# Performance work log

Hardware: AMD Instinct MI355X
Metric: run time of the kernel (lower is better)

The kernel has to match this reference:

```python
import jax, jax.numpy as jnp
import numpy as np

D = 2048
G = 16


def setup_inputs() -> dict:
    key = jax.random.key(0)
    ks = jax.random.split(key, 7)
    scale = 1.0 / np.sqrt(D)
    x = jax.random.normal(ks[0], (4, 4096, D), dtype=jnp.float32)
    Wq = jax.random.uniform(ks[1], (D, D), jnp.float32, -scale, scale)
    bq = jax.random.uniform(ks[2], (D,), jnp.float32, -scale, scale)
    Wk = jax.random.uniform(ks[3], (D, D), jnp.float32, -scale, scale)
    bk = jax.random.uniform(ks[4], (D,), jnp.float32, -scale, scale)
    Wv = jax.random.uniform(ks[5], (D, D), jnp.float32, -scale, scale)
    bv = jax.random.uniform(ks[6], (D,), jnp.float32, -scale, scale)
    return {"x": x, "Wq": Wq, "bq": bq, "Wk": Wk, "bk": bk, "Wv": Wv, "bv": bv}


def reference(x, Wq, bq, Wk, bk, Wv, bv):
    B, T, Df = x.shape
    g = G
    d = Df // g  # per-group dim = 128
    q = x @ Wq.T + bq
    k = x @ Wk.T + bk
    v = x @ Wv.T + bv
    qs = q.reshape(B, T, g, d)
    ks_ = k.reshape(B, T, g, d)
    vs = v.reshape(B, T, g, d)
    # attention over the GROUP axis per token: scores are (B,T,g,g)
    scores = jnp.einsum('btgd,bthd->btgh', qs, ks_) / jnp.sqrt(jnp.asarray(d, x.dtype))
    att = jax.nn.softmax(scores, axis=-1)
    out = jnp.einsum('btgh,bthd->btgd', att, vs)
    return out.reshape(B, T, Df)
```

## Files before the change

kernel.cpp:

```cpp
#include <hip/hip_runtime.h>


#define DIM 2048
#define NTOT 6144
#define DG 128
#define NG 16
#define BK 64
#define KT64 (DIM / BK)

typedef __bf16 bf16x8 __attribute__((ext_vector_type(8)));
typedef float f32x4 __attribute__((ext_vector_type(4)));
typedef unsigned short u16;
typedef unsigned int u32;

__device__ __forceinline__ u16 f2bf(float f) {
  u32 u = __float_as_uint(f);
  u = (u + 0x7fffu + ((u >> 16) & 1u)) >> 16;
  return (u16)u;
}

__device__ __forceinline__ void gload16(const __bf16* g, __bf16* l) {
  __builtin_amdgcn_global_load_lds(
      (__attribute__((address_space(1))) void*)(void*)g,
      (__attribute__((address_space(3))) void*)l, 16, 0, 0);
}

__global__ __launch_bounds__(256) void cvt_kernel(const float* __restrict__ src,
                                                  u16* __restrict__ dst, int n4) {
  int i = blockIdx.x * 256 + threadIdx.x;
  if (i >= n4) return;
  float4 f = ((const float4*)src)[i];
  ushort4 o;
  o.x = f2bf(f.x); o.y = f2bf(f.y); o.z = f2bf(f.z); o.w = f2bf(f.w);
  ((ushort4*)dst)[i] = o;
}

__global__ __launch_bounds__(256) void cvtW_kernel(const float* __restrict__ wq,
                                                   const float* __restrict__ wk,
                                                   const float* __restrict__ wv,
                                                   u16* __restrict__ dst, int n4each) {
  int m = blockIdx.y;
  const float* s = (m == 0) ? wq : (m == 1) ? wk : wv;
  int i = blockIdx.x * 256 + threadIdx.x;
  if (i >= n4each) return;
  float4 f = ((const float4*)s)[i];
  ushort4 o;
  o.x = f2bf(f.x); o.y = f2bf(f.y); o.z = f2bf(f.z); o.w = f2bf(f.w);
  ((ushort4*)dst)[(size_t)m * n4each + i] = o;
}

__global__ __launch_bounds__(512, 1) void gemm_qkv(const __bf16* __restrict__ A,
                                                   const __bf16* __restrict__ W,
                                                   const float* __restrict__ bq,
                                                   const float* __restrict__ bk,
                                                   const float* __restrict__ bv,
                                                   u16* __restrict__ C) {
  __shared__ __bf16 lds[2 * 32768];

  const int tid = threadIdx.x;
  const int lane = tid & 63;
  const int w = tid >> 6;
  const int wm = w >> 2, wn = w & 3;
  const int lm = lane & 15, kq = lane >> 4;

  const int bid = blockIdx.x;
  const int swz = (bid & 7) * 192 + (bid >> 3);
  const int bm = swz % 64;
  const int bn = swz / 64;

  const int srow = tid >> 3;
  const int scol = ((tid & 7) ^ ((tid >> 3) & 7)) * 8;
  const __bf16* pA = A + (size_t)(bm * 256 + srow) * DIM + scol;
  const __bf16* pB = W + (size_t)(bn * 256 + srow) * DIM + scol;

#define STAGEH(tt, p)                                                         \
  {                                                                           \
    __bf16* db = lds + ((tt) & 1) * 32768 + ((p) >> 1) * 16384 +              \
                 ((p) & 1) * 8192 + tid * 8;                                  \
    const __bf16* sp = (((p) >> 1) == 0 ? pA : pB) +                          \
                       (size_t)(((p) & 1) * 128) * DIM + (size_t)(tt) * BK;   \
    gload16(sp, db);                                                          \
    gload16(sp + (size_t)64 * DIM, db + 4096);                                \
  }

  f32x4 acc[8][4];
#pragma unroll
  for (int i = 0; i < 8; ++i)
#pragma unroll
    for (int j = 0; j < 4; ++j) acc[i][j] = (f32x4){0.f, 0.f, 0.f, 0.f};

  int aoff[2][2], boff[2][2];
#pragma unroll
  for (int ih = 0; ih < 2; ++ih)
#pragma unroll
    for (int kk = 0; kk < 2; ++kk)
      aoff[ih][kk] = (wm * 128 + ih * 64 + lm) * 64 + (((kk << 2) | kq) ^ (lm & 7)) * 8;
#pragma unroll
  for (int jh = 0; jh < 2; ++jh)
#pragma unroll
    for (int kk = 0; kk < 2; ++kk)
      boff[jh][kk] = (wn * 64 + jh * 32 + lm) * 64 + (((kk << 2) | kq) ^ (lm & 7)) * 8;

  bf16x8 af[4][2], bfr[2][2];

#define PH(tv, ih, jh, dostage, p)                                            \
  {                                                                           \
    const __bf16* bufb = lds + ((tv) & 1) * 32768;                            \
    if ((jh) == 0) {                                                          \
      _Pragma("unroll") for (int ir = 0; ir < 4; ++ir)                        \
        _Pragma("unroll") for (int kk = 0; kk < 2; ++kk)                      \
          af[ir][kk] = *(const bf16x8*)(bufb + aoff[ih][kk] + ir * 1024);     \
    }                                                                         \
    _Pragma("unroll") for (int jr = 0; jr < 2; ++jr)                          \
      _Pragma("unroll") for (int kk = 0; kk < 2; ++kk)                        \
        bfr[jr][kk] = *(const bf16x8*)(bufb + 16384 + boff[jh][kk] + jr * 1024); \
    if (dostage) STAGEH((tv) + 1, p);                                         \
    __builtin_amdgcn_sched_barrier(0);                                       \
    asm volatile("s_barrier" ::: "memory");                                   \
    asm volatile("s_waitcnt lgkmcnt(0)" ::: "memory");                        \
    __builtin_amdgcn_sched_barrier(0);                                       \
    __builtin_amdgcn_s_setprio(1);                                            \
    _Pragma("unroll") for (int ir = 0; ir < 4; ++ir)                          \
      _Pragma("unroll") for (int jr = 0; jr < 2; ++jr)                        \
        _Pragma("unroll") for (int kk = 0; kk < 2; ++kk)                      \
          acc[(ih) * 4 + ir][(jh) * 2 + jr] =                                 \
              __builtin_amdgcn_mfma_f32_16x16x32_bf16(                        \
                  af[ir][kk], bfr[jr][kk], acc[(ih) * 4 + ir][(jh) * 2 + jr], \
                  0, 0, 0);                                                   \
    __builtin_amdgcn_s_setprio(0);                                            \
    if ((p) == 3) asm volatile("s_waitcnt vmcnt(0)" ::: "memory");            \
    asm volatile("s_barrier" ::: "memory");                                   \
  }

  STAGEH(0, 0) STAGEH(0, 1) STAGEH(0, 2) STAGEH(0, 3)
  asm volatile("s_waitcnt vmcnt(0)" ::: "memory");
  asm volatile("s_barrier" ::: "memory");

#pragma unroll 1
  for (int t = 0; t < KT64 - 1; ++t) {
    PH(t, 0, 0, 1, 0)
    PH(t, 0, 1, 1, 1)
    PH(t, 1, 0, 1, 2)
    PH(t, 1, 1, 1, 3)
  }
  PH(KT64 - 1, 0, 0, 0, 0)
  PH(KT64 - 1, 0, 1, 0, 1)
  PH(KT64 - 1, 1, 0, 0, 2)
  PH(KT64 - 1, 1, 1, 0, 3)
#undef PH
#undef STAGEH

  const int mat = bn >> 3;
  const float* bias = (mat == 0) ? bq : (mat == 1) ? bk : bv;
  const int colb = bn * 256 + wn * 64 + lm;
  const int rowb = bm * 256 + wm * 128 + kq * 4;
#pragma unroll
  for (int i = 0; i < 8; ++i) {
#pragma unroll
    for (int j = 0; j < 4; ++j) {
      const int col = colb + j * 16;
      const float bs = bias[col & (DIM - 1)];
#pragma unroll
      for (int r = 0; r < 4; ++r) {
        const int row = rowb + i * 16 + r;
        C[(size_t)row * NTOT + col] = f2bf(acc[i][j][r] + bs);
      }
    }
  }
}

__device__ __forceinline__ void unpack8(uint4 v, float* f) {
  f[0] = __uint_as_float(v.x << 16);
  f[1] = __uint_as_float(v.x & 0xffff0000u);
  f[2] = __uint_as_float(v.y << 16);
  f[3] = __uint_as_float(v.y & 0xffff0000u);
  f[4] = __uint_as_float(v.z << 16);
  f[5] = __uint_as_float(v.z & 0xffff0000u);
  f[6] = __uint_as_float(v.w << 16);
  f[7] = __uint_as_float(v.w & 0xffff0000u);
}

__global__ __launch_bounds__(256) void attn_kernel(const u16* __restrict__ qkv,
                                                   float* __restrict__ out) {
  __shared__ __bf16 kv[4][4096];

  const int tid = threadIdx.x;
  const int lane = tid & 63;
  const int w = tid >> 6;
  const int token = blockIdx.x * 4 + w;
  const int g = lane & 15, s = lane >> 4;

  const __bf16* base = (const __bf16*)(qkv) + (size_t)token * NTOT;

  const __bf16* kvsrc = base + DIM;
#pragma unroll
  for (int i = 0; i < 8; ++i)
    gload16(kvsrc + i * 512 + lane * 8, (__bf16*)kv[w] + i * 512);

  float qf[32];
  const __bf16* qsrc = base + g * DG + s * 32;
#pragma unroll
  for (int j = 0; j < 4; ++j) {
    uint4 qc = *(const uint4*)(qsrc + j * 8);
    unpack8(qc, qf + j * 8);
  }

  asm volatile("s_waitcnt vmcnt(0)" ::: "memory");

  float sc[16];
  const __bf16* kl = (const __bf16*)kv[w] + s * 32;
#pragma unroll 4
  for (int h = 0; h < 16; ++h) {
    const uint4* kr = (const uint4*)(kl + h * DG);
    float a = 0.f;
#pragma unroll
    for (int j = 0; j < 4; ++j) {
      float kf[8];
      unpack8(kr[j], kf);
#pragma unroll
      for (int e = 0; e < 8; ++e) a = fmaf(qf[j * 8 + e], kf[e], a);
    }
    sc[h] = a;
  }
#pragma unroll
  for (int h = 0; h < 16; ++h) {
    float v = sc[h];
    v += __shfl_xor(v, 16);
    v += __shfl_xor(v, 32);
    sc[h] = v;
  }

  const float scale = 0.08838834764831845f;
  float mx = sc[0] * scale;
#pragma unroll
  for (int h = 1; h < 16; ++h) mx = fmaxf(mx, sc[h] * scale);
  float p[16], sum = 0.f;
#pragma unroll
  for (int h = 0; h < 16; ++h) {
    p[h] = __expf(sc[h] * scale - mx);
    sum += p[h];
  }
  const float inv = 1.f / sum;
#pragma unroll
  for (int h = 0; h < 16; ++h) p[h] *= inv;

  float o[32];
#pragma unroll
  for (int e = 0; e < 32; ++e) o[e] = 0.f;
  const __bf16* vl = (const __bf16*)kv[w] + 2048 + s * 32;
#pragma unroll 4
  for (int h = 0; h < 16; ++h) {
    const uint4* vr = (const uint4*)(vl + h * DG);
    const float ph = p[h];
#pragma unroll
    for (int j = 0; j < 4; ++j) {
      float vf[8];
      unpack8(vr[j], vf);
#pragma unroll
      for (int e = 0; e < 8; ++e) o[j * 8 + e] = fmaf(ph, vf[e], o[j * 8 + e]);
    }
  }

  float* ob = out + (size_t)token * DIM + g * DG + s * 32;
#pragma unroll
  for (int j = 0; j < 8; ++j) {
    float4 v4 = {o[j * 4], o[j * 4 + 1], o[j * 4 + 2], o[j * 4 + 3]};
    ((float4*)ob)[j] = v4;
  }
}

extern "C" void kernel_launch(void* const* d_in, const int* in_sizes, int n_in,
                              void* d_out, int out_size, void* d_ws, size_t ws_size,
                              hipStream_t stream) {
  const float* x  = (const float*)d_in[0];
  const float* Wq = (const float*)d_in[1];
  const float* bq = (const float*)d_in[2];
  const float* Wk = (const float*)d_in[3];
  const float* bk = (const float*)d_in[4];
  const float* Wv = (const float*)d_in[5];
  const float* bv = (const float*)d_in[6];
  float* out = (float*)d_out;

  const int M = in_sizes[0] / DIM;

  u16* xb  = (u16*)d_ws;
  u16* wb  = xb + (size_t)M * DIM;
  u16* qkv = wb + (size_t)3 * DIM * DIM;

  const int n4x = (M * DIM) / 4;
  cvt_kernel<<<dim3((n4x + 255) / 256), 256, 0, stream>>>(x, xb, n4x);
  const int n4w = (DIM * DIM) / 4;
  cvtW_kernel<<<dim3((n4w + 255) / 256, 3), 256, 0, stream>>>(Wq, Wk, Wv, wb, n4w);

  gemm_qkv<<<dim3((M / 256) * (NTOT / 256)), 512, 0, stream>>>(
      (const __bf16*)xb, (const __bf16*)wb, bq, bk, bv, qkv);

  attn_kernel<<<dim3(M / 4), 256, 0, stream>>>(qkv, out);
}
```

Measured before the change: 719.7 us.

## Split LDS tiles into K-halves to wait on partial loads earlier

Restructures the QKV GEMM's shared-memory staging so each 64-wide K tile is stored as two 32-wide halves (A and B each), with a new XOR swizzle for 32-element rows. Each phase now handles one K-half and one row half with the full 4x4 MFMA set. The loop waits with vmcnt(4) instead of vmcnt(0), so compute on the first K-half can start while the second half is still in flight. The intent is finer-grained overlap of global-to-LDS copies with MFMA. The vmcnt bookkeeping is delicate, and the wait count and swizzle must match the load order exactly.

```diff
diff --git a/kernel.cpp b/kernel.cpp
--- a/kernel.cpp
+++ b/kernel.cpp
@@ -68,19 +68,17 @@
   const int bm = swz % 64;
   const int bn = swz / 64;
 
-  const int srow = tid >> 3;
-  const int scol = ((tid & 7) ^ ((tid >> 3) & 7)) * 8;
-  const __bf16* pA = A + (size_t)(bm * 256 + srow) * DIM + scol;
-  const __bf16* pB = W + (size_t)(bn * 256 + srow) * DIM + scol;
-
-#define STAGEH(tt, p)                                                         \
+  const int scol = ((tid & 3) ^ ((tid >> 3) & 3)) * 8;
+  const __bf16* pA = A + (size_t)(bm * 256 + (tid >> 2)) * DIM + scol;
+  const __bf16* pB = W + (size_t)(bn * 256 + (tid >> 2)) * DIM + scol;
+
+#define STAGEH(tt, kk, isB)                                                   \
   {                                                                           \
-    __bf16* db = lds + ((tt) & 1) * 32768 + ((p) >> 1) * 16384 +              \
-                 ((p) & 1) * 8192 + tid * 8;                                  \
-    const __bf16* sp = (((p) >> 1) == 0 ? pA : pB) +                          \
-                       (size_t)(((p) & 1) * 128) * DIM + (size_t)(tt) * BK;   \
+    __bf16* db = lds + ((tt) & 1) * 32768 + ((kk) * 2 + (isB)) * 8192 +       \
+                 tid * 8;                                                     \
+    const __bf16* sp = ((isB) ? pB : pA) + (size_t)(tt) * BK + (kk) * 32;     \
     gload16(sp, db);                                                          \
-    gload16(sp + (size_t)64 * DIM, db + 4096);                                \
+    gload16(sp + (size_t)128 * DIM, db + 4096);                               \
   }
 
   f32x4 acc[8][4];
@@ -89,64 +87,52 @@
 #pragma unroll
     for (int j = 0; j < 4; ++j) acc[i][j] = (f32x4){0.f, 0.f, 0.f, 0.f};
 
-  int aoff[2][2], boff[2][2];
-#pragma unroll
-  for (int ih = 0; ih < 2; ++ih)
-#pragma unroll
-    for (int kk = 0; kk < 2; ++kk)
-      aoff[ih][kk] = (wm * 128 + ih * 64 + lm) * 64 + (((kk << 2) | kq) ^ (lm & 7)) * 8;
-#pragma unroll
-  for (int jh = 0; jh < 2; ++jh)
-#pragma unroll
-    for (int kk = 0; kk < 2; ++kk)
-      boff[jh][kk] = (wn * 64 + jh * 32 + lm) * 64 + (((kk << 2) | kq) ^ (lm & 7)) * 8;
-
-  bf16x8 af[4][2], bfr[2][2];
-
-#define PH(tv, ih, jh, dostage, p)                                            \
+  const int sw = (kq ^ ((lm >> 1) & 3)) * 8;
+  const int aoff = (wm * 128 + lm) * 32 + sw;
+  const int boff = (wn * 64 + lm) * 32 + sw;
+
+  bf16x8 af[4], bf[4];
+
+#define PH(tv, kk, ih, dostage, vmN)                                          \
   {                                                                           \
-    const __bf16* bufb = lds + ((tv) & 1) * 32768;                            \
-    if ((jh) == 0) {                                                          \
-      _Pragma("unroll") for (int ir = 0; ir < 4; ++ir)                        \
-        _Pragma("unroll") for (int kk = 0; kk < 2; ++kk)                      \
-          af[ir][kk] = *(const bf16x8*)(bufb + aoff[ih][kk] + ir * 1024);     \
+    const __bf16* bufb = lds + ((tv) & 1) * 32768 + (kk) * 16384;             \
+    _Pragma("unroll") for (int ir = 0; ir < 4; ++ir)                          \
+      af[ir] = *(const bf16x8*)(bufb + aoff + ((ih) * 4 + ir) * 512);         \
+    if ((ih) == 0) {                                                          \
+      _Pragma("unroll") for (int jr = 0; jr < 4; ++jr)                        \
+        bf[jr] = *(const bf16x8*)(bufb + 8192 + boff + jr * 512);             \
     }                                                                         \
-    _Pragma("unroll") for (int jr = 0; jr < 2; ++jr)                          \
-      _Pragma("unroll") for (int kk = 0; kk < 2; ++kk)                        \
-        bfr[jr][kk] = *(const bf16x8*)(bufb + 16384 + boff[jh][kk] + jr * 1024); \
-    if (dostage) STAGEH((tv) + 1, p);                                         \
-    __builtin_amdgcn_sched_barrier(0);                                       \
+    if (dostage) STAGEH((tv) + 1, kk, ih)                                     \
+    __builtin_amdgcn_sched_barrier(0);                                        \
     asm volatile("s_barrier" ::: "memory");                                   \
     asm volatile("s_waitcnt lgkmcnt(0)" ::: "memory");                        \
-    __builtin_amdgcn_sched_barrier(0);                                       \
+    __builtin_amdgcn_sched_barrier(0);                                        \
     __builtin_amdgcn_s_setprio(1);                                            \
     _Pragma("unroll") for (int ir = 0; ir < 4; ++ir)                          \
-      _Pragma("unroll") for (int jr = 0; jr < 2; ++jr)                        \
-        _Pragma("unroll") for (int kk = 0; kk < 2; ++kk)                      \
-          acc[(ih) * 4 + ir][(jh) * 2 + jr] =                                 \
-              __builtin_amdgcn_mfma_f32_16x16x32_bf16(                        \
-                  af[ir][kk], bfr[jr][kk], acc[(ih) * 4 + ir][(jh) * 2 + jr], \
-                  0, 0, 0);                                                   \
+      _Pragma("unroll") for (int jr = 0; jr < 4; ++jr)                        \
+        acc[(ih) * 4 + ir][jr] = __builtin_amdgcn_mfma_f32_16x16x32_bf16(     \
+            af[ir], bf[jr], acc[(ih) * 4 + ir][jr], 0, 0, 0);                 \
     __builtin_amdgcn_s_setprio(0);                                            \
-    if ((p) == 3) asm volatile("s_waitcnt vmcnt(0)" ::: "memory");            \
+    if ((vmN) == 4) asm volatile("s_waitcnt vmcnt(4)" ::: "memory");          \
+    if ((vmN) == 0) asm volatile("s_waitcnt vmcnt(0)" ::: "memory");          \
     asm volatile("s_barrier" ::: "memory");                                   \
   }
 
-  STAGEH(0, 0) STAGEH(0, 1) STAGEH(0, 2) STAGEH(0, 3)
-  asm volatile("s_waitcnt vmcnt(0)" ::: "memory");
+  STAGEH(0, 0, 0) STAGEH(0, 0, 1) STAGEH(0, 1, 0) STAGEH(0, 1, 1)
+  asm volatile("s_waitcnt vmcnt(4)" ::: "memory");
   asm volatile("s_barrier" ::: "memory");
 
 #pragma unroll 1
   for (int t = 0; t < KT64 - 1; ++t) {
-    PH(t, 0, 0, 1, 0)
-    PH(t, 0, 1, 1, 1)
-    PH(t, 1, 0, 1, 2)
-    PH(t, 1, 1, 1, 3)
-  }
-  PH(KT64 - 1, 0, 0, 0, 0)
-  PH(KT64 - 1, 0, 1, 0, 1)
-  PH(KT64 - 1, 1, 0, 0, 2)
-  PH(KT64 - 1, 1, 1, 0, 3)
+    PH(t, 0, 0, 1, -1)
+    PH(t, 0, 1, 1, 4)
+    PH(t, 1, 0, 1, -1)
+    PH(t, 1, 1, 1, 4)
+  }
+  PH(KT64 - 1, 0, 0, 0, -1)
+  PH(KT64 - 1, 0, 1, 0, 0)
+  PH(KT64 - 1, 1, 0, 0, -1)
+  PH(KT64 - 1, 1, 1, 0, -1)
 #undef PH
 #undef STAGEH
 
```

Measured after the change: 713.9 us. About the same (-0.8%).
